# Performance work log

Measured on AMD Instinct MI355X. Metric: run time of the kernel, lower is better.

The kernel has to match this reference:

```python
import jax, jax.numpy as jnp
import numpy as np

N = 20000      # nodes
E = 320000     # edges
IN = 300       # input_channel
HID = 100      # hidden_channel (= heads*out_channels with heads=1)
R = 50         # num_relations
B = 8          # num_bases (the 4th positional arg 'heads'=8 lands on num_bases in PyG RGATConv)
HEADS = 1
CLS = 3
Q = 64         # number of query (aspect) nodes
EPS = 1e-16


def setup_inputs() -> dict:
    key = jax.random.key(0)
    ks = jax.random.split(key, 16)
    x = jax.random.normal(ks[0], (N, IN), jnp.float32)
    edge_index = jax.random.randint(ks[1], (2, E), 0, N)
    edge_type = jax.random.randint(ks[2], (E,), 0, R)
    query_indices = jax.random.randint(ks[3], (Q,), 0, N)

    def w(k, shape, scale):
        return jax.random.normal(k, shape, jnp.float32) * scale

    comp1 = w(ks[4], (R, B), 0.3)
    basis1 = w(ks[5], (B, IN, HEADS * HID), 1.0 / np.sqrt(IN))
    q1 = w(ks[6], (HEADS * HID, HEADS), 0.1)
    k1 = w(ks[7], (HEADS * HID, HEADS), 0.1)
    b1 = jnp.zeros((HEADS * HID,), jnp.float32)
    comp2 = w(ks[8], (R, B), 0.3)
    basis2 = w(ks[9], (B, HID, HEADS * HID), 1.0 / np.sqrt(HID))
    q2 = w(ks[10], (HEADS * HID, HEADS), 0.1)
    k2 = w(ks[11], (HEADS * HID, HEADS), 0.1)
    b2 = jnp.zeros((HEADS * HID,), jnp.float32)
    Wl = w(ks[12], (CLS, HID), 1.0 / np.sqrt(HID))
    bl = jnp.zeros((CLS,), jnp.float32)
    return dict(x=x, edge_index=edge_index, edge_type=edge_type,
                query_indices=query_indices,
                comp1=comp1, basis1=basis1, q1=q1, k1=k1, b1=b1,
                comp2=comp2, basis2=basis2, q2=q2, k2=k2, b2=b2,
                Wl=Wl, bl=bl)


def segment_softmax(alpha, seg, num_segments):
    # numerically-stable softmax over edges grouped by destination node
    m = jax.ops.segment_max(alpha, seg, num_segments=num_segments)  # [N, H]
    e = jnp.exp(alpha - m[seg])
    s = jax.ops.segment_sum(e, seg, num_segments=num_segments)
    return e / (s[seg] + EPS)


def rgat_conv(x, edge_index, edge_type, comp, basis, q, k, b):
    # basis-decomposed per-relation weight: [R, in, H*out]
    W = jnp.einsum('rb,bio->rio', comp, basis)
    # transform every node under every relation once, then gather per edge
    xt = jnp.einsum('ni,rio->nro', x, W)          # [N, R, H*out]
    src, dst = edge_index[0], edge_index[1]        # j -> i (source_to_target)
    xi = xt[dst, edge_type]                        # [E, H*out]
    xj = xt[src, edge_type]                        # [E, H*out]
    qi = xi @ q                                    # [E, H]
    kj = xj @ k                                    # [E, H]
    alpha = jax.nn.leaky_relu(qi + kj, 0.2)        # additive self-attention
    alpha = segment_softmax(alpha, dst, N)         # across-relation softmax
    msg = xj.reshape(E, HEADS, HID) * alpha[:, :, None]
    out = jax.ops.segment_sum(msg, dst, num_segments=N)  # [N, H, out]
    return out.reshape(N, HEADS * HID) + b         # concat=True


def reference(x, edge_index, edge_type, query_indices,
              comp1, basis1, q1, k1, b1,
              comp2, basis2, q2, k2, b2, Wl, bl):
    h = jax.nn.relu(rgat_conv(x, edge_index, edge_type, comp1, basis1, q1, k1, b1))
    h = jax.nn.relu(rgat_conv(h, edge_index, edge_type, comp2, basis2, q2, k2, b2))
    pooled = h[query_indices].mean(axis=0)          # [HID]
    return pooled @ Wl.T + bl                       # [CLS]
```

## Files before the change

### kernel.cpp

```cpp
#include <hip/hip_runtime.h>
#include <math.h>

#define N_NODES 20000
#define E_EDGES 320000
#define IN_CH   300
#define HID     100
#define R_REL   50
#define NB      8
#define CLS     3
#define NQ      64
#define OUTW    800
#define ZW      100
#define SCAN_BLKS ((N_NODES + 255) / 256)

typedef unsigned short ushort_t;
typedef __attribute__((ext_vector_type(8))) short     short8;
typedef __attribute__((ext_vector_type(8))) unsigned short ushort8;
typedef __attribute__((ext_vector_type(4))) float     f32x4;
typedef __attribute__((ext_vector_type(2))) float     f32x2;

__device__ __forceinline__ ushort_t f2bf_rne(float f) {
    unsigned u = __float_as_uint(f);
    unsigned r = (u + 0x7fffu + ((u >> 16) & 1u)) >> 16;
    return (ushort_t)r;
}
__device__ __forceinline__ float bf2f(ushort_t u) {
    return __uint_as_float((unsigned)u << 16);
}

__global__ __launch_bounds__(256) void zero_deg2(int* __restrict__ dd,
                                                 int* __restrict__ ds) {
    int i = blockIdx.x * 256 + threadIdx.x;
    if (i < N_NODES) { dd[i] = 0; ds[i] = 0; }
}

__global__ __launch_bounds__(256) void hist2_kernel(
        const int* __restrict__ ei, int* __restrict__ dd,
        int* __restrict__ ds) {
    int e = blockIdx.x * 256 + threadIdx.x;
    if (e < E_EDGES) {
        atomicAdd(&dd[ei[E_EDGES + e]], 1);
        atomicAdd(&ds[ei[e]], 1);
    }
}

__global__ __launch_bounds__(256) void scan1_both(
        const int* __restrict__ deg_d, int* __restrict__ rp_d, int* __restrict__ bsum_d,
        const int* __restrict__ deg_s, int* __restrict__ rp_s, int* __restrict__ bsum_s) {
    int set = blockIdx.x / SCAN_BLKS, blk = blockIdx.x % SCAN_BLKS;
    const int* deg = set ? deg_s : deg_d;
    int* rowptr    = set ? rp_s  : rp_d;
    int* bsum      = set ? bsum_s : bsum_d;
    __shared__ int s[256];
    int tid = threadIdx.x;
    int idx = blk * 256 + tid;
    int v = (idx < N_NODES) ? deg[idx] : 0;
    s[tid] = v; __syncthreads();
    #pragma unroll
    for (int off = 1; off < 256; off <<= 1) {
        int t = (tid >= off) ? s[tid - off] : 0;
        __syncthreads();
        s[tid] += t;
        __syncthreads();
    }
    if (idx < N_NODES) rowptr[idx] = s[tid] - v;
    if (tid == 255) bsum[blk] = s[255];
}

__global__ __launch_bounds__(128) void scan2_both(
        int* __restrict__ bsum_d, int* __restrict__ rp_d,
        int* __restrict__ bsum_s, int* __restrict__ rp_s) {
    int* bsum   = blockIdx.x ? bsum_s : bsum_d;
    int* rowptr = blockIdx.x ? rp_s   : rp_d;
    __shared__ int s[128];
    int tid = threadIdx.x;
    int v = (tid < SCAN_BLKS) ? bsum[tid] : 0;
    s[tid] = v; __syncthreads();
    #pragma unroll
    for (int off = 1; off < 128; off <<= 1) {
        int t = (tid >= off) ? s[tid - off] : 0;
        __syncthreads();
        s[tid] += t;
        __syncthreads();
    }
    if (tid < SCAN_BLKS) bsum[tid] = s[tid] - v;
    if (tid == 0) rowptr[N_NODES] = E_EDGES;
}

__global__ __launch_bounds__(256) void scan3_both(
        int* __restrict__ rp_d, const int* __restrict__ bsum_d, int* __restrict__ cur_d,
        int* __restrict__ rp_s, const int* __restrict__ bsum_s, int* __restrict__ cur_s) {
    int set = blockIdx.x / SCAN_BLKS, blk = blockIdx.x % SCAN_BLKS;
    int* rowptr      = set ? rp_s   : rp_d;
    const int* bsum  = set ? bsum_s : bsum_d;
    int* cursor      = set ? cur_s  : cur_d;
    int idx = blk * 256 + threadIdx.x;
    if (idx < N_NODES) {
        int v = rowptr[idx] + bsum[blk];
        rowptr[idx] = v;
        cursor[idx] = v;
    }
}

__global__ __launch_bounds__(256) void scatter_both(
        const int* __restrict__ ei, const int* __restrict__ et,
        int* __restrict__ cur_d, int* __restrict__ cur_s,
        int* __restrict__ skey, int* __restrict__ skey_s,
        int* __restrict__ zidx) {
    int e = blockIdx.x * 256 + threadIdx.x;
    if (e >= E_EDGES) return;
    int s = ei[e], d = ei[E_EDGES + e], rt = et[e];
    int p = atomicAdd(&cur_d[d], 1);
    skey[p] = (s << 6) | rt;
    int qp = atomicAdd(&cur_s[s], 1);
    skey_s[qp] = rt;
    zidx[p] = qp;
}

__global__ __launch_bounds__(256) void prep_kernel(
        const float* __restrict__ basis, const float* __restrict__ q,
        const float* __restrict__ k, ushort_t* __restrict__ Bt,
        float* __restrict__ qb, float* __restrict__ kb,
        int K, int Kp, int split_blocks) {
    int bx = blockIdx.x;
    if (bx < split_blocks) {
        int idx = bx * 256 + threadIdx.x;
        if (idx >= OUTW * Kp) return;
        int n = idx / Kp, kk = idx - n * Kp;
        int b = n / HID, o = n - b * HID;
        float v = 0.f;
        if (kk < K) v = basis[((size_t)b * K + kk) * HID + o];
        Bt[idx] = f2bf_rne(v);
    } else {
        int idx = (bx - split_blocks) * 256 + threadIdx.x;
        if (idx >= K * NB) return;
        int kk = idx >> 3, b = idx & 7;
        const float* br = basis + ((size_t)b * K + kk) * HID;
        float aq = 0.f, ak = 0.f;
        for (int o = 0; o < HID; o++) {
            float v = br[o];
            aq = fmaf(v, q[o], aq);
            ak = fmaf(v, k[o], ak);
        }
        qb[idx] = aq; kb[idx] = ak;
    }
}

#define BM 32
#define BN 160
__global__ __launch_bounds__(256) void gemm_mfma(
        const float* __restrict__ A, const ushort_t* __restrict__ Bt,
        ushort_t* __restrict__ xbh, int M, int K, int Kp, int do_relu) {
    __shared__ ushort_t As[BM * 328];
    __shared__ ushort_t Bs[BN * 32];
    int tid  = threadIdx.x;
    int lane = tid & 63, wave = tid >> 6;
    int ml = lane & 15, quad = lane >> 4;
    int wr = (wave >> 1) * 16, wc = (wave & 1) * 80;
    int row0 = blockIdx.x * BM;
    int col0 = blockIdx.y * BN;
    int SW = Kp + 8;
    int ksteps = Kp >> 5;

    {
        int ra = tid >> 3;
        int gr = row0 + ra;
        const float* ar = A + (size_t)gr * K;
        for (int c = (tid & 7); c * 8 < Kp; c += 8) {
            int kb = c * 8;
            float vals[8];
            if (gr < M) {
                if (kb + 8 <= K) {
                    float4 f0 = *(const float4*)&ar[kb];
                    float4 f1 = *(const float4*)&ar[kb + 4];
                    vals[0]=f0.x; vals[1]=f0.y; vals[2]=f0.z; vals[3]=f0.w;
                    vals[4]=f1.x; vals[5]=f1.y; vals[6]=f1.z; vals[7]=f1.w;
                } else {
                    #pragma unroll
                    for (int i = 0; i < 8; i++)
                        vals[i] = (kb + i < K) ? ar[kb + i] : 0.f;
                }
                if (do_relu)
                    #pragma unroll
                    for (int i = 0; i < 8; i++) vals[i] = fmaxf(vals[i], 0.f);
            } else {
                #pragma unroll
                for (int i = 0; i < 8; i++) vals[i] = 0.f;
            }
            ushort8 hv;
            #pragma unroll
            for (int i = 0; i < 8; i++) hv[i] = f2bf_rne(vals[i]);
            *(ushort8*)&As[ra * SW + kb] = hv;
        }
    }

    f32x4 acc[5] = {};
    for (int ks = 0; ks < ksteps; ks++) {
        int k0 = ks << 5;
        __syncthreads();
        for (int t = tid; t < 640; t += 256) {
            int rb = t >> 2, ch = t & 3;
            __builtin_amdgcn_global_load_lds(
                (const __attribute__((address_space(1))) unsigned int*)
                    &Bt[(size_t)(col0 + rb) * Kp + k0 + ch * 8],
                (__attribute__((address_space(3))) unsigned int*)&Bs[t * 8],
                16, 0, 0);
        }
        __syncthreads();
        short8 af, bf[5];
        af = *(const short8*)&As[(wr + ml) * SW + k0 + quad * 8];
        #pragma unroll
        for (int nt = 0; nt < 5; nt++)
            bf[nt] = *(const short8*)&Bs[(wc + nt * 16 + ml) * 32 + quad * 8];
        #pragma unroll
        for (int nt = 0; nt < 5; nt++)
            acc[nt] = __builtin_amdgcn_mfma_f32_16x16x32_bf16(af, bf[nt], acc[nt], 0, 0, 0);
    }
    #pragma unroll
    for (int nt = 0; nt < 5; nt++) {
        #pragma unroll
        for (int r = 0; r < 4; r++) {
            int grow = row0 + wr + quad * 4 + r;
            if (grow < M)
                xbh[(size_t)grow * OUTW + col0 + wc + nt * 16 + ml] =
                    f2bf_rne(acc[nt][r]);
        }
    }
}

__global__ __launch_bounds__(256) void qk2_kernel(
        const float* __restrict__ x, const float* __restrict__ qb,
        const float* __restrict__ kb, float* __restrict__ xbq,
        float* __restrict__ xbk, int K, int do_relu) {
    __shared__ float sqb[320 * NB], skb[320 * NB];
    int tid = threadIdx.x;
    for (int i = tid; i < K * NB; i += 256) { sqb[i] = qb[i]; skb[i] = kb[i]; }
    __syncthreads();
    int idx = blockIdx.x * 256 + tid;
    if (idx >= N_NODES * NB) return;
    int n = idx >> 3, b = idx & 7;
    const float* xr = x + (size_t)n * K;
    float aq = 0.f, ak = 0.f;
    for (int kk = 0; kk < K; kk++) {
        float v = xr[kk];
        if (do_relu) v = fmaxf(v, 0.f);
        aq = fmaf(v, sqb[kk * NB + b], aq);
        ak = fmaf(v, skb[kk * NB + b], ak);
    }
    xbq[idx] = aq;
    xbk[idx] = ak;
}

__global__ __launch_bounds__(256) void compute_z(
        const int* __restrict__ rowptr_s, const int* __restrict__ skey_s,
        const float* __restrict__ comp, const ushort_t* __restrict__ xbh,
        ushort_t* __restrict__ Z) {
    int wave = threadIdx.x >> 6, lane = threadIdx.x & 63;
    int s = blockIdx.x * 4 + wave;
    if (s >= N_NODES) return;
    int beg = rowptr_s[s], end = rowptr_s[s + 1];
    if (beg == end) return;
    int o = lane * 2;
    f32x2 xrow[NB];
    if (lane < 50) {
        #pragma unroll
        for (int b = 0; b < NB; b++) {
            ushort2 xx = *(const ushort2*)&xbh[(size_t)s * OUTW + b * HID + o];
            xrow[b].x = bf2f(xx.x);
            xrow[b].y = bf2f(xx.y);
        }
    }
    for (int p = beg; p < end; p++) {
        int rt = skey_s[p] & 63;
        const float* cr = comp + rt * NB;
        if (lane < 50) {
            f32x2 z = {0.f, 0.f};
            #pragma unroll
            for (int b = 0; b < NB; b++) z += cr[b] * xrow[b];
            ushort2 zz;
            zz.x = f2bf_rne(z.x);
            zz.y = f2bf_rne(z.y);
            *(ushort2*)&Z[(size_t)p * ZW + o] = zz;
        }
    }
}

__global__ __launch_bounds__(256) void msg_soft(
        const int* __restrict__ rowptr, const int* __restrict__ skey,
        const int* __restrict__ zidx,
        const float* __restrict__ comp, const ushort_t* __restrict__ Z,
        const float* __restrict__ xbq, const float* __restrict__ xbk,
        const float* __restrict__ bias, float* __restrict__ h) {
    int wave = threadIdx.x >> 6, lane = threadIdx.x & 63;
    int d = blockIdx.x * 4 + wave;
    if (d >= N_NODES) return;
    int beg = rowptr[d], end = rowptr[d + 1];

    float4 qd0 = *(const float4*)&xbq[d * NB];
    float4 qd1 = *(const float4*)&xbq[d * NB + 4];

    f32x2 acc = {0.f, 0.f};
    float m = -1e30f, l = 0.f;
    int o = lane * 2;

    for (int c0 = beg; c0 < end; c0 += 64) {
        int p = c0 + lane;
        bool valid = p < end;
        float a = -1e30f;
        int zi = 0;
        if (valid) {
            int key = skey[p];
            zi = zidx[p];
            int s = key >> 6, rt = key & 63;
            const float4 c0v = *(const float4*)&comp[rt * NB];
            const float4 c1v = *(const float4*)&comp[rt * NB + 4];
            const float4 k0v = *(const float4*)&xbk[s * NB];
            const float4 k1v = *(const float4*)&xbk[s * NB + 4];
            float qi = c0v.x*qd0.x + c0v.y*qd0.y + c0v.z*qd0.z + c0v.w*qd0.w
                     + c1v.x*qd1.x + c1v.y*qd1.y + c1v.z*qd1.z + c1v.w*qd1.w;
            float kj = c0v.x*k0v.x + c0v.y*k0v.y + c0v.z*k0v.z + c0v.w*k0v.w
                     + c1v.x*k1v.x + c1v.y*k1v.y + c1v.z*k1v.z + c1v.w*k1v.w;
            a = qi + kj;
            a = a > 0.f ? a : 0.2f * a;
        }
        float cm = a;
        #pragma unroll
        for (int off = 32; off; off >>= 1) cm = fmaxf(cm, __shfl_xor(cm, off));
        float M = fmaxf(m, cm);
        float scale = __expf(m - M);
        acc *= scale; l *= scale; m = M;
        float wgt = valid ? __expf(a - M) : 0.f;
        float cs = wgt;
        #pragma unroll
        for (int off = 32; off; off >>= 1) cs += __shfl_xor(cs, off);
        l += cs;
        int cnt = end - c0; if (cnt > 64) cnt = 64;
        for (int j = 0; j < cnt; j++) {
            float wj = __shfl(wgt, j);
            int   zj = __shfl(zi, j);
            if (lane < 50) {
                ushort2 zz = *(const ushort2*)&Z[(size_t)zj * ZW + o];
                f32x2 zv = {bf2f(zz.x), bf2f(zz.y)};
                acc += wj * zv;
            }
        }
    }
    if (lane < 50) {
        float inv = 1.f / (l + 1e-16f);
        f32x2 r;
        r.x = bias[o]     + acc.x * inv;
        r.y = bias[o + 1] + acc.y * inv;
        *(f32x2*)&h[(size_t)d * HID + o] = r;
    }
}

__global__ __launch_bounds__(128) void head_kernel(
        const float* __restrict__ h2, const int* __restrict__ qidx,
        const float* __restrict__ Wl, const float* __restrict__ bl,
        float* __restrict__ out) {
    __shared__ float pooled[HID];
    int tid = threadIdx.x;
    if (tid < HID) {
        float s = 0.f;
        for (int i = 0; i < NQ; i++)
            s += fmaxf(h2[(size_t)qidx[i] * HID + tid], 0.f);
        pooled[tid] = s * (1.0f / NQ);
    }
    __syncthreads();
    if (tid < CLS) {
        float s = bl[tid];
        for (int o = 0; o < HID; o++) s = fmaf(pooled[o], Wl[tid * HID + o], s);
        out[tid] = s;
    }
}

extern "C" void kernel_launch(void* const* d_in, const int* in_sizes, int n_in,
                              void* d_out, int out_size, void* d_ws, size_t ws_size,
                              hipStream_t stream) {
    const float* x      = (const float*)d_in[0];
    const int*   ei     = (const int*)  d_in[1];
    const int*   et     = (const int*)  d_in[2];
    const int*   qidx   = (const int*)  d_in[3];
    const float* comp1  = (const float*)d_in[4];
    const float* basis1 = (const float*)d_in[5];
    const float* q1     = (const float*)d_in[6];
    const float* k1     = (const float*)d_in[7];
    const float* b1     = (const float*)d_in[8];
    const float* comp2  = (const float*)d_in[9];
    const float* basis2 = (const float*)d_in[10];
    const float* q2     = (const float*)d_in[11];
    const float* k2     = (const float*)d_in[12];
    const float* b2     = (const float*)d_in[13];
    const float* Wl     = (const float*)d_in[14];
    const float* bl     = (const float*)d_in[15];
    float* out = (float*)d_out;

    const int KP1 = 320, KP2 = 128;

    char* w = (char*)d_ws;
    size_t off = 0;
    auto alloc = [&](size_t nbytes) {
        void* p = (void*)(w + off);
        off += ((nbytes + 255) / 256) * 256;
        return p;
    };
    ushort_t* xbh    = (ushort_t*)alloc((size_t)N_NODES * OUTW * 2);
    ushort_t* Z      = (ushort_t*)alloc((size_t)E_EDGES * ZW * 2);
    float*    h1     = (float*)alloc((size_t)N_NODES * HID * 4);
    float*    h2     = (float*)alloc((size_t)N_NODES * HID * 4);
    ushort_t* Bt     = (ushort_t*)alloc((size_t)OUTW * KP1 * 2);
    float*    xbq    = (float*)alloc((size_t)N_NODES * NB * 4);
    float*    xbk    = (float*)alloc((size_t)N_NODES * NB * 4);
    float*    qb     = (float*)alloc((size_t)KP1 * NB * 4);
    float*    kb     = (float*)alloc((size_t)KP1 * NB * 4);
    int*      deg_d  = (int*)alloc(N_NODES * 4);
    int*      deg_s  = (int*)alloc(N_NODES * 4);
    int*      rp_d   = (int*)alloc((N_NODES + 1) * 4);
    int*      rp_s   = (int*)alloc((N_NODES + 1) * 4);
    int*      cur_d  = (int*)alloc(N_NODES * 4);
    int*      cur_s  = (int*)alloc(N_NODES * 4);
    int*      bsum_d = (int*)alloc(SCAN_BLKS * 4);
    int*      bsum_s = (int*)alloc(SCAN_BLKS * 4);
    int*      skey   = (int*)alloc(E_EDGES * 4);
    int*      skey_s = (int*)alloc(E_EDGES * 4);
    int*      zidx   = (int*)alloc(E_EDGES * 4);

    zero_deg2<<<SCAN_BLKS, 256, 0, stream>>>(deg_d, deg_s);
    hist2_kernel<<<(E_EDGES + 255) / 256, 256, 0, stream>>>(ei, deg_d, deg_s);
    scan1_both<<<2 * SCAN_BLKS, 256, 0, stream>>>(deg_d, rp_d, bsum_d, deg_s, rp_s, bsum_s);
    scan2_both<<<2, 128, 0, stream>>>(bsum_d, rp_d, bsum_s, rp_s);
    scan3_both<<<2 * SCAN_BLKS, 256, 0, stream>>>(rp_d, bsum_d, cur_d, rp_s, bsum_s, cur_s);
    scatter_both<<<(E_EDGES + 255) / 256, 256, 0, stream>>>(ei, et, cur_d, cur_s, skey, skey_s, zidx);

    auto layer = [&](const float* input, int K, int Kp, int relu_in,
                     const float* comp, const float* basis, const float* q,
                     const float* k, const float* bias, float* hout) {
        int split_blocks = (OUTW * Kp + 255) / 256;
        int qb_blocks = (K * NB + 255) / 256;
        prep_kernel<<<split_blocks + qb_blocks, 256, 0, stream>>>(
            basis, q, k, Bt, qb, kb, K, Kp, split_blocks);
        dim3 g((N_NODES + BM - 1) / BM, OUTW / BN);
        gemm_mfma<<<g, 256, 0, stream>>>(input, Bt, xbh, N_NODES, K, Kp, relu_in);
        qk2_kernel<<<(N_NODES * NB + 255) / 256, 256, 0, stream>>>(input, qb, kb, xbq, xbk, K, relu_in);
        compute_z<<<(N_NODES + 3) / 4, 256, 0, stream>>>(rp_s, skey_s, comp, xbh, Z);
        msg_soft<<<(N_NODES + 3) / 4, 256, 0, stream>>>(rp_d, skey, zidx, comp, Z, xbq, xbk, bias, hout);
    };

    layer(x,  IN_CH, KP1, 0, comp1, basis1, q1, k1, b1, h1);
    layer(h1, HID,   KP2, 1, comp2, basis2, q2, k2, b2, h2);
    head_kernel<<<1, 128, 0, stream>>>(h2, qidx, Wl, bl, out);
}
```

Before: 412.7 us.

## Loop all column blocks per GEMM block with double-buffered per-wave B loads; compute qk from xbh

The GEMM grid drops its column dimension. Each block now converts its A tile to bf16 once and walks all five column blocks, prefetching per-wave B fragments into double-buffered LDS with global_load_lds and waitcnt instead of block-wide barriers. The q/k projection now reads the bf16 xbh output, which removes the qb/kb precompute and the pass over the fp32 input. The cost is fewer blocks (one per 32 rows), more LDS per block, and q/k scores computed from bf16-rounded values.

```diff
diff --git a/kernel.cpp b/kernel.cpp
--- a/kernel.cpp
+++ b/kernel.cpp
@@ -117,50 +117,34 @@
     zidx[p] = qp;
 }
 
-__global__ __launch_bounds__(256) void prep_kernel(
-        const float* __restrict__ basis, const float* __restrict__ q,
-        const float* __restrict__ k, ushort_t* __restrict__ Bt,
-        float* __restrict__ qb, float* __restrict__ kb,
-        int K, int Kp, int split_blocks) {
-    int bx = blockIdx.x;
-    if (bx < split_blocks) {
-        int idx = bx * 256 + threadIdx.x;
-        if (idx >= OUTW * Kp) return;
-        int n = idx / Kp, kk = idx - n * Kp;
-        int b = n / HID, o = n - b * HID;
-        float v = 0.f;
-        if (kk < K) v = basis[((size_t)b * K + kk) * HID + o];
-        Bt[idx] = f2bf_rne(v);
-    } else {
-        int idx = (bx - split_blocks) * 256 + threadIdx.x;
-        if (idx >= K * NB) return;
-        int kk = idx >> 3, b = idx & 7;
-        const float* br = basis + ((size_t)b * K + kk) * HID;
-        float aq = 0.f, ak = 0.f;
-        for (int o = 0; o < HID; o++) {
-            float v = br[o];
-            aq = fmaf(v, q[o], aq);
-            ak = fmaf(v, k[o], ak);
-        }
-        qb[idx] = aq; kb[idx] = ak;
-    }
+__global__ __launch_bounds__(256) void split_bt_kernel(
+        const float* __restrict__ basis, ushort_t* __restrict__ Bt,
+        int K, int Kp) {
+    int idx = blockIdx.x * 256 + threadIdx.x;
+    if (idx >= OUTW * Kp) return;
+    int n = idx / Kp, k = idx - n * Kp;
+    int b = n / HID, o = n - b * HID;
+    float v = 0.f;
+    if (k < K) v = basis[((size_t)b * K + k) * HID + o];
+    Bt[idx] = f2bf_rne(v);
 }
 
 #define BM 32
 #define BN 160
+#define NCB (OUTW / BN)
 __global__ __launch_bounds__(256) void gemm_mfma(
         const float* __restrict__ A, const ushort_t* __restrict__ Bt,
         ushort_t* __restrict__ xbh, int M, int K, int Kp, int do_relu) {
     __shared__ ushort_t As[BM * 328];
-    __shared__ ushort_t Bs[BN * 32];
+    __shared__ ushort_t Bs[2 * 4 * 2560];
     int tid  = threadIdx.x;
     int lane = tid & 63, wave = tid >> 6;
     int ml = lane & 15, quad = lane >> 4;
     int wr = (wave >> 1) * 16, wc = (wave & 1) * 80;
     int row0 = blockIdx.x * BM;
-    int col0 = blockIdx.y * BN;
     int SW = Kp + 8;
     int ksteps = Kp >> 5;
+    int T = NCB * ksteps;
 
     {
         int ra = tid >> 3;
@@ -193,59 +177,81 @@
             *(ushort8*)&As[ra * SW + kb] = hv;
         }
     }
-
-    f32x4 acc[5] = {};
-    for (int ks = 0; ks < ksteps; ks++) {
+    __syncthreads();
+
+    ushort_t* bsw = &Bs[wave * 2560];
+    auto issue = [&](int t) {
+        int cb = t / ksteps, ks = t - cb * ksteps;
+        int col0 = cb * BN + wc;
         int k0 = ks << 5;
-        __syncthreads();
-        for (int t = tid; t < 640; t += 256) {
-            int rb = t >> 2, ch = t & 3;
+        ushort_t* dst = bsw + (t & 1) * 10240;
+        #pragma unroll
+        for (int nt = 0; nt < 5; nt++) {
             __builtin_amdgcn_global_load_lds(
                 (const __attribute__((address_space(1))) unsigned int*)
-                    &Bt[(size_t)(col0 + rb) * Kp + k0 + ch * 8],
-                (__attribute__((address_space(3))) unsigned int*)&Bs[t * 8],
+                    &Bt[(size_t)(col0 + nt * 16 + ml) * Kp + k0 + quad * 8],
+                (__attribute__((address_space(3))) unsigned int*)
+                    &dst[nt * 512 + lane * 8],
                 16, 0, 0);
         }
-        __syncthreads();
-        short8 af, bf[5];
-        af = *(const short8*)&As[(wr + ml) * SW + k0 + quad * 8];
-        #pragma unroll
-        for (int nt = 0; nt < 5; nt++)
-            bf[nt] = *(const short8*)&Bs[(wc + nt * 16 + ml) * 32 + quad * 8];
-        #pragma unroll
-        for (int nt = 0; nt < 5; nt++)
-            acc[nt] = __builtin_amdgcn_mfma_f32_16x16x32_bf16(af, bf[nt], acc[nt], 0, 0, 0);
-    }
-    #pragma unroll
-    for (int nt = 0; nt < 5; nt++) {
-        #pragma unroll
-        for (int r = 0; r < 4; r++) {
-            int grow = row0 + wr + quad * 4 + r;
-            if (grow < M)
-                xbh[(size_t)grow * OUTW + col0 + wc + nt * 16 + ml] =
-                    f2bf_rne(acc[nt][r]);
-        }
-    }
-}
-
-__global__ __launch_bounds__(256) void qk2_kernel(
-        const float* __restrict__ x, const float* __restrict__ qb,
-        const float* __restrict__ kb, float* __restrict__ xbq,
-        float* __restrict__ xbk, int K, int do_relu) {
-    __shared__ float sqb[320 * NB], skb[320 * NB];
+    };
+
+    f32x4 acc[5] = {};
+    issue(0);
+    for (int t = 0; t < T; t++) {
+        int cb = t / ksteps, ks = t - cb * ksteps;
+        int k0 = ks << 5;
+        if (t + 1 < T) {
+            issue(t + 1);
+            __builtin_amdgcn_s_waitcnt(0x0F75);
+        } else {
+            __builtin_amdgcn_s_waitcnt(0x0F70);
+        }
+        const ushort_t* src = bsw + (t & 1) * 10240;
+        short8 af = *(const short8*)&As[(wr + ml) * SW + k0 + quad * 8];
+        #pragma unroll
+        for (int nt = 0; nt < 5; nt++) {
+            short8 bfv = *(const short8*)&src[nt * 512 + lane * 8];
+            acc[nt] = __builtin_amdgcn_mfma_f32_16x16x32_bf16(af, bfv, acc[nt], 0, 0, 0);
+        }
+        if (ks == ksteps - 1) {
+            int col0 = cb * BN;
+            #pragma unroll
+            for (int nt = 0; nt < 5; nt++) {
+                #pragma unroll
+                for (int r = 0; r < 4; r++) {
+                    int grow = row0 + wr + quad * 4 + r;
+                    if (grow < M)
+                        xbh[(size_t)grow * OUTW + col0 + wc + nt * 16 + ml] =
+                            f2bf_rne(acc[nt][r]);
+                }
+                acc[nt] = (f32x4){0.f, 0.f, 0.f, 0.f};
+            }
+        }
+    }
+}
+
+__global__ __launch_bounds__(256) void qk3_kernel(
+        const ushort_t* __restrict__ xbh, const float* __restrict__ q,
+        const float* __restrict__ k, float* __restrict__ xbq,
+        float* __restrict__ xbk) {
+    __shared__ float sq[HID], sk[HID];
     int tid = threadIdx.x;
-    for (int i = tid; i < K * NB; i += 256) { sqb[i] = qb[i]; skb[i] = kb[i]; }
+    if (tid < HID) { sq[tid] = q[tid]; sk[tid] = k[tid]; }
     __syncthreads();
     int idx = blockIdx.x * 256 + tid;
     if (idx >= N_NODES * NB) return;
-    int n = idx >> 3, b = idx & 7;
-    const float* xr = x + (size_t)n * K;
+    const ushort_t* xr = xbh + (size_t)(idx >> 3) * OUTW + (idx & 7) * HID;
     float aq = 0.f, ak = 0.f;
-    for (int kk = 0; kk < K; kk++) {
-        float v = xr[kk];
-        if (do_relu) v = fmaxf(v, 0.f);
-        aq = fmaf(v, sqb[kk * NB + b], aq);
-        ak = fmaf(v, skb[kk * NB + b], ak);
+    #pragma unroll
+    for (int c = 0; c < 25; c++) {
+        ushort4 v = *(const ushort4*)&xr[c * 4];
+        #pragma unroll
+        for (int i = 0; i < 4; i++) {
+            float f = bf2f(((const ushort_t*)&v)[i]);
+            aq = fmaf(f, sq[c * 4 + i], aq);
+            ak = fmaf(f, sk[c * 4 + i], ak);
+        }
     }
     xbq[idx] = aq;
     xbk[idx] = ak;
@@ -411,8 +417,6 @@
     ushort_t* Bt     = (ushort_t*)alloc((size_t)OUTW * KP1 * 2);
     float*    xbq    = (float*)alloc((size_t)N_NODES * NB * 4);
     float*    xbk    = (float*)alloc((size_t)N_NODES * NB * 4);
-    float*    qb     = (float*)alloc((size_t)KP1 * NB * 4);
-    float*    kb     = (float*)alloc((size_t)KP1 * NB * 4);
     int*      deg_d  = (int*)alloc(N_NODES * 4);
     int*      deg_s  = (int*)alloc(N_NODES * 4);
     int*      rp_d   = (int*)alloc((N_NODES + 1) * 4);
@@ -435,13 +439,10 @@
     auto layer = [&](const float* input, int K, int Kp, int relu_in,
                      const float* comp, const float* basis, const float* q,
                      const float* k, const float* bias, float* hout) {
-        int split_blocks = (OUTW * Kp + 255) / 256;
-        int qb_blocks = (K * NB + 255) / 256;
-        prep_kernel<<<split_blocks + qb_blocks, 256, 0, stream>>>(
-            basis, q, k, Bt, qb, kb, K, Kp, split_blocks);
-        dim3 g((N_NODES + BM - 1) / BM, OUTW / BN);
-        gemm_mfma<<<g, 256, 0, stream>>>(input, Bt, xbh, N_NODES, K, Kp, relu_in);
-        qk2_kernel<<<(N_NODES * NB + 255) / 256, 256, 0, stream>>>(input, qb, kb, xbq, xbk, K, relu_in);
+        int nb = OUTW * Kp;
+        split_bt_kernel<<<(nb + 255) / 256, 256, 0, stream>>>(basis, Bt, K, Kp);
+        gemm_mfma<<<(N_NODES + BM - 1) / BM, 256, 0, stream>>>(input, Bt, xbh, N_NODES, K, Kp, relu_in);
+        qk3_kernel<<<(N_NODES * NB + 255) / 256, 256, 0, stream>>>(xbh, q, k, xbq, xbk);
         compute_z<<<(N_NODES + 3) / 4, 256, 0, stream>>>(rp_s, skey_s, comp, xbh, Z);
         msg_soft<<<(N_NODES + 3) / 4, 256, 0, stream>>>(rp_d, skey, zidx, comp, Z, xbq, xbk, bias, hout);
     };
```

Result: slower. 494.2 us (+19.7%).
